# Performance work log

Measured on AMD Instinct MI355X. Metric: run time of the kernel, lower is better.

The kernel has to match this reference:

```python
import jax, jax.numpy as jnp
import numpy as np

B, CW_DIM = 256, 8192
DIM_EMBED = 128
DICT_SIZE = 4096
DIM_CODES = CW_DIM // DIM_EMBED  # 64


def setup_inputs() -> dict:
    key = jax.random.key(0)
    k1, k2 = jax.random.split(key)
    x = jax.random.normal(k1, (B, CW_DIM), dtype=jnp.float32)
    dictionary = jax.random.normal(k2, (DIM_CODES, DICT_SIZE, DIM_EMBED), dtype=jnp.float32)
    return {"x": x, "dictionary": dictionary}


def reference(x, dictionary):
    """VQVAE.quantise (eval mode): pairwise sq-distance -> argmin -> gather + one-hot.

    x: [B, cw_dim], dictionary: [C, S, E] with cw_dim = C*E.
    Returns (cw_embed [B, C*E], one_hot_idx [B, C, S]).
    """
    Bb, D = x.shape
    C, S, E = dictionary.shape
    xr = x.reshape(Bb, C, E)                                   # [B, C, E]
    x_sq = jnp.sum(xr * xr, axis=-1, keepdims=True)            # [B, C, 1]
    d_sq = jnp.sum(dictionary * dictionary, axis=-1)           # [C, S]
    cross = jnp.einsum('bce,cse->bcs', xr, dictionary)         # [B, C, S] (GEMM)
    dist = x_sq + d_sq[None, :, :] - 2.0 * cross               # [B, C, S]
    idx = jnp.argmin(dist, axis=-1)                            # [B, C]
    # gather nearest codes: dictionary[c, idx[b,c]] -> [B, C, E]
    code_ids = jnp.arange(C)[None, :]                          # [1, C]
    cw_embed = dictionary[code_ids, idx]                       # [B, C, E]
    cw_embed = cw_embed.reshape(Bb, C * E)                     # [B, cw_dim]
    one_hot_idx = jax.nn.one_hot(idx, S, dtype=x.dtype)        # [B, C, S]
    return cw_embed, one_hot_idx
```

## Files before the change

kernel.cpp:

```cpp
#include <hip/hip_runtime.h>
#include <stdint.h>


#define B_SZ 256
#define C_SZ 64
#define E_SZ 128
#define S_SZ 4096
#define CW   8192
#define LDB  136

typedef __attribute__((ext_vector_type(4))) float    float4a;
typedef __attribute__((ext_vector_type(8))) _Float16 half8;

__device__ __forceinline__ void split8(float4a f0, float4a f1, half8& hi, half8& lo) {
    #pragma unroll
    for (int j = 0; j < 4; ++j) {
        _Float16 h0 = (_Float16)f0[j];
        hi[j]     = h0;
        lo[j]     = (_Float16)(f0[j] - (float)h0);
        _Float16 h1 = (_Float16)f1[j];
        hi[4 + j] = h1;
        lo[4 + j] = (_Float16)(f1[j] - (float)h1);
    }
}

__global__ __launch_bounds__(512, 2) void argmin_mfma(
    const float* __restrict__ x,
    const float* __restrict__ dict,
    int* __restrict__ idx_out,
    float* __restrict__ cw_out)
{
    __shared__ __attribute__((aligned(16))) _Float16 bh[128 * LDB];
    __shared__ __attribute__((aligned(16))) _Float16 bl[128 * LDB];
    __shared__ float4a dsqp[128];
    __shared__ int     fid[64];
    float* rv = reinterpret_cast<float*>(bh);
    int*   ri = reinterpret_cast<int*>(bl);

    const int tid   = threadIdx.x;
    const int lane  = tid & 63;
    const int quad  = lane >> 4;
    const int l15   = lane & 15;
    const int wid   = tid >> 6;
    const int mhalf = wid & 1;
    const int nquad = wid >> 1;
    const int c     = blockIdx.x & 63;
    const int btile = blockIdx.x >> 6;

    int m_attr[4], n_attr[4];
    {
        half8 ones, enc;
        #pragma unroll
        for (int j = 0; j < 8; ++j) { ones[j] = (_Float16)1.0f; enc[j] = (_Float16)(float)l15; }
        float4a z = {0.f, 0.f, 0.f, 0.f};
        float4a pr = __builtin_amdgcn_mfma_f32_16x16x32_f16(enc, ones, z, 0, 0, 0);
        float4a pc = __builtin_amdgcn_mfma_f32_16x16x32_f16(ones, enc, z, 0, 0, 0);
        #pragma unroll
        for (int r = 0; r < 4; ++r) {
            m_attr[r] = (int)(pr[r] * 0.03125f + 0.5f);
            n_attr[r] = (int)(pc[r] * 0.03125f + 0.5f);
        }
    }

    half8 ah[2][4], al[2][4];
    #pragma unroll
    for (int mi = 0; mi < 2; ++mi) {
        int b = btile * 64 + mhalf * 32 + mi * 16 + l15;
        const float* xr = x + (size_t)b * CW + c * E_SZ;
        #pragma unroll
        for (int kk = 0; kk < 4; ++kk) {
            float4a f0 = *reinterpret_cast<const float4a*>(xr + kk * 32 + quad * 8);
            float4a f1 = *reinterpret_cast<const float4a*>(xr + kk * 32 + quad * 8 + 4);
            split8(f0, f1, ah[mi][kk], al[mi][kk]);
        }
    }

    float bestv[8];
    int   besti[8];
    #pragma unroll
    for (int i = 0; i < 8; ++i) { bestv[i] = 3.4e38f; besti[i] = 0; }

    for (int s0 = 0; s0 < S_SZ; s0 += 128) {
        __syncthreads();
        {
            int srow = tid >> 2;
            int kq   = (tid & 3) * 32;
            const float* dr = dict + ((size_t)c * S_SZ + (s0 + srow)) * E_SZ + kq;
            float dp = 0.f;
            #pragma unroll
            for (int ck = 0; ck < 4; ++ck) {
                float4a f0 = *reinterpret_cast<const float4a*>(dr + ck * 8);
                float4a f1 = *reinterpret_cast<const float4a*>(dr + ck * 8 + 4);
                half8 h, l;
                split8(f0, f1, h, l);
                #pragma unroll
                for (int j = 0; j < 4; ++j) { dp = fmaf(f0[j], f0[j], dp); dp = fmaf(f1[j], f1[j], dp); }
                *reinterpret_cast<half8*>(bh + srow * LDB + kq + ck * 8) = h;
                *reinterpret_cast<half8*>(bl + srow * LDB + kq + ck * 8) = l;
            }
            dsqp[srow][tid & 3] = dp;
        }
        __syncthreads();

        half8 bhf[2][4], blf[2][4];
        #pragma unroll
        for (int ni = 0; ni < 2; ++ni) {
            int sl = nquad * 32 + ni * 16 + l15;
            #pragma unroll
            for (int kk = 0; kk < 4; ++kk) {
                bhf[ni][kk] = *reinterpret_cast<const half8*>(bh + sl * LDB + kk * 32 + quad * 8);
                blf[ni][kk] = *reinterpret_cast<const half8*>(bl + sl * LDB + kk * 32 + quad * 8);
            }
        }

        float4a acc[2][2] = {{{0.f,0.f,0.f,0.f},{0.f,0.f,0.f,0.f}},
                             {{0.f,0.f,0.f,0.f},{0.f,0.f,0.f,0.f}}};
        #pragma unroll
        for (int kk = 0; kk < 4; ++kk)
            #pragma unroll
            for (int mi = 0; mi < 2; ++mi)
                #pragma unroll
                for (int ni = 0; ni < 2; ++ni) {
                    acc[mi][ni] = __builtin_amdgcn_mfma_f32_16x16x32_f16(
                        ah[mi][kk], bhf[ni][kk], acc[mi][ni], 0, 0, 0);
                    acc[mi][ni] = __builtin_amdgcn_mfma_f32_16x16x32_f16(
                        ah[mi][kk], blf[ni][kk], acc[mi][ni], 0, 0, 0);
                    acc[mi][ni] = __builtin_amdgcn_mfma_f32_16x16x32_f16(
                        al[mi][kk], bhf[ni][kk], acc[mi][ni], 0, 0, 0);
                }

        #pragma unroll
        for (int ni = 0; ni < 2; ++ni)
            #pragma unroll
            for (int r = 0; r < 4; ++r) {
                int sl = nquad * 32 + ni * 16 + n_attr[r];
                float4a q4 = dsqp[sl];
                float dsq = (q4[0] + q4[1]) + (q4[2] + q4[3]);
                int sg = s0 + sl;
                #pragma unroll
                for (int mi = 0; mi < 2; ++mi) {
                    float dist = dsq - 2.0f * acc[mi][ni][r];
                    int slot = mi * 4 + r;
                    if (dist < bestv[slot]) { bestv[slot] = dist; besti[slot] = sg; }
                }
            }
    }

    __syncthreads();

    #pragma unroll
    for (int mi = 0; mi < 2; ++mi)
        #pragma unroll
        for (int r = 0; r < 4; ++r) {
            int row = mhalf * 32 + mi * 16 + m_attr[r];
            int col = nquad * 16 + n_attr[r];
            rv[row * 64 + col] = bestv[mi * 4 + r];
            ri[row * 64 + col] = besti[mi * 4 + r];
        }
    __syncthreads();

    if (tid < 64) {
        float bv = 3.4e38f; int bi = 0x7fffffff;
        for (int j = 0; j < 64; ++j) {
            float v = rv[tid * 64 + j];
            int   i = ri[tid * 64 + j];
            if (v < bv || (v == bv && i < bi)) { bv = v; bi = i; }
        }
        idx_out[(btile * 64 + tid) * C_SZ + c] = bi;
        fid[tid] = bi;
    }
    __syncthreads();

    for (int u = tid; u < 64 * 32; u += 512) {
        int row = u >> 5, ch = u & 31;
        int bi = fid[row];
        float4a v = *reinterpret_cast<const float4a*>(
            dict + ((size_t)c * S_SZ + bi) * E_SZ + ch * 4);
        *reinterpret_cast<float4a*>(
            cw_out + (size_t)(btile * 64 + row) * CW + c * E_SZ + ch * 4) = v;
    }
}

__global__ void scatter_ones(const int* __restrict__ idx, float* __restrict__ oh) {
    int r = blockIdx.x * 256 + threadIdx.x;
    oh[(size_t)r * S_SZ + idx[r]] = 1.0f;
}

extern "C" void kernel_launch(void* const* d_in, const int* in_sizes, int n_in,
                              void* d_out, int out_size, void* d_ws, size_t ws_size,
                              hipStream_t stream) {
    const float* x    = (const float*)d_in[0];
    const float* dict = (const float*)d_in[1];
    float* out = (float*)d_out;
    int* idx = (int*)d_ws;
    float* oh = out + (size_t)B_SZ * CW;

    hipMemsetAsync(oh, 0, (size_t)B_SZ * C_SZ * S_SZ * sizeof(float), stream);
    argmin_mfma<<<dim3(256), dim3(512), 0, stream>>>(x, dict, idx, out);
    scatter_ones<<<dim3(B_SZ * C_SZ / 256), dim3(256), 0, stream>>>(idx, oh);
}
```

Before: 486.6 us.

## Double-buffer dictionary tiles in LDS and fuse one-hot fill into one kernel

The argmin kernel now double-buffers the fp16 hi/lo dictionary tiles in shared memory. It prefetches the next tile's global loads into registers before the MFMA work on the current tile, then splits and stores them afterwards, so each iteration needs one barrier instead of two. B-fragment loads move inside the k loop to cut register pressure. Separately, the memset plus scatter is replaced by a single kernel that writes the whole one-hot row with nontemporal vector stores, avoiding a second pass over the 256 MB output. The cost is doubled LDS use, which may reduce occupancy, and more registers held by the prefetch.

```diff
diff --git a/kernel.cpp b/kernel.cpp
--- a/kernel.cpp
+++ b/kernel.cpp
@@ -30,9 +30,9 @@
     int* __restrict__ idx_out,
     float* __restrict__ cw_out)
 {
-    __shared__ __attribute__((aligned(16))) _Float16 bh[128 * LDB];
-    __shared__ __attribute__((aligned(16))) _Float16 bl[128 * LDB];
-    __shared__ float4a dsqp[128];
+    __shared__ __attribute__((aligned(16))) _Float16 bh[2][128 * LDB];
+    __shared__ __attribute__((aligned(16))) _Float16 bl[2][128 * LDB];
+    __shared__ float4a dsqp[2][128];
     __shared__ int     fid[64];
     float* rv = reinterpret_cast<float*>(bh);
     int*   ri = reinterpret_cast<int*>(bl);
@@ -75,67 +75,87 @@
         }
     }
 
+    const int srow = tid >> 2;
+    const int kq   = (tid & 3) * 32;
+    const int q4   = tid & 3;
+    const float* drow = dict + ((size_t)c * S_SZ + srow) * E_SZ + kq;
+
+    float4a pf0[4], pf1[4];
+    #pragma unroll
+    for (int ck = 0; ck < 4; ++ck) {
+        pf0[ck] = *reinterpret_cast<const float4a*>(drow + ck * 8);
+        pf1[ck] = *reinterpret_cast<const float4a*>(drow + ck * 8 + 4);
+    }
+    {
+        float dp = 0.f;
+        #pragma unroll
+        for (int ck = 0; ck < 4; ++ck) {
+            half8 h, l;
+            split8(pf0[ck], pf1[ck], h, l);
+            #pragma unroll
+            for (int j = 0; j < 4; ++j) {
+                dp = fmaf(pf0[ck][j], pf0[ck][j], dp);
+                dp = fmaf(pf1[ck][j], pf1[ck][j], dp);
+            }
+            *reinterpret_cast<half8*>(&bh[0][srow * LDB + kq + ck * 8]) = h;
+            *reinterpret_cast<half8*>(&bl[0][srow * LDB + kq + ck * 8]) = l;
+        }
+        dsqp[0][srow][q4] = dp;
+    }
+
     float bestv[8];
     int   besti[8];
     #pragma unroll
     for (int i = 0; i < 8; ++i) { bestv[i] = 3.4e38f; besti[i] = 0; }
 
-    for (int s0 = 0; s0 < S_SZ; s0 += 128) {
-        __syncthreads();
-        {
-            int srow = tid >> 2;
-            int kq   = (tid & 3) * 32;
-            const float* dr = dict + ((size_t)c * S_SZ + (s0 + srow)) * E_SZ + kq;
-            float dp = 0.f;
+    __syncthreads();
+
+    int cur = 0;
+    for (int it = 0; it < 32; ++it) {
+        const int s0 = it * 128;
+
+        if (it + 1 < 32) {
+            const float* dr = drow + (size_t)(it + 1) * (128 * E_SZ);
             #pragma unroll
             for (int ck = 0; ck < 4; ++ck) {
-                float4a f0 = *reinterpret_cast<const float4a*>(dr + ck * 8);
-                float4a f1 = *reinterpret_cast<const float4a*>(dr + ck * 8 + 4);
-                half8 h, l;
-                split8(f0, f1, h, l);
-                #pragma unroll
-                for (int j = 0; j < 4; ++j) { dp = fmaf(f0[j], f0[j], dp); dp = fmaf(f1[j], f1[j], dp); }
-                *reinterpret_cast<half8*>(bh + srow * LDB + kq + ck * 8) = h;
-                *reinterpret_cast<half8*>(bl + srow * LDB + kq + ck * 8) = l;
-            }
-            dsqp[srow][tid & 3] = dp;
-        }
-        __syncthreads();
-
-        half8 bhf[2][4], blf[2][4];
-        #pragma unroll
-        for (int ni = 0; ni < 2; ++ni) {
-            int sl = nquad * 32 + ni * 16 + l15;
-            #pragma unroll
-            for (int kk = 0; kk < 4; ++kk) {
-                bhf[ni][kk] = *reinterpret_cast<const half8*>(bh + sl * LDB + kk * 32 + quad * 8);
-                blf[ni][kk] = *reinterpret_cast<const half8*>(bl + sl * LDB + kk * 32 + quad * 8);
-            }
-        }
-
+                pf0[ck] = *reinterpret_cast<const float4a*>(dr + ck * 8);
+                pf1[ck] = *reinterpret_cast<const float4a*>(dr + ck * 8 + 4);
+            }
+        }
+
+        const _Float16* bhc = bh[cur];
+        const _Float16* blc = bl[cur];
         float4a acc[2][2] = {{{0.f,0.f,0.f,0.f},{0.f,0.f,0.f,0.f}},
                              {{0.f,0.f,0.f,0.f},{0.f,0.f,0.f,0.f}}};
         #pragma unroll
-        for (int kk = 0; kk < 4; ++kk)
+        for (int kk = 0; kk < 4; ++kk) {
+            half8 bhf[2], blf[2];
+            #pragma unroll
+            for (int ni = 0; ni < 2; ++ni) {
+                const int sl = nquad * 32 + ni * 16 + l15;
+                bhf[ni] = *reinterpret_cast<const half8*>(bhc + sl * LDB + kk * 32 + quad * 8);
+                blf[ni] = *reinterpret_cast<const half8*>(blc + sl * LDB + kk * 32 + quad * 8);
+            }
             #pragma unroll
             for (int mi = 0; mi < 2; ++mi)
                 #pragma unroll
                 for (int ni = 0; ni < 2; ++ni) {
                     acc[mi][ni] = __builtin_amdgcn_mfma_f32_16x16x32_f16(
-                        ah[mi][kk], bhf[ni][kk], acc[mi][ni], 0, 0, 0);
+                        ah[mi][kk], bhf[ni], acc[mi][ni], 0, 0, 0);
                     acc[mi][ni] = __builtin_amdgcn_mfma_f32_16x16x32_f16(
-                        ah[mi][kk], blf[ni][kk], acc[mi][ni], 0, 0, 0);
+                        ah[mi][kk], blf[ni], acc[mi][ni], 0, 0, 0);
                     acc[mi][ni] = __builtin_amdgcn_mfma_f32_16x16x32_f16(
-                        al[mi][kk], bhf[ni][kk], acc[mi][ni], 0, 0, 0);
+                        al[mi][kk], bhf[ni], acc[mi][ni], 0, 0, 0);
                 }
+        }
 
         #pragma unroll
         for (int ni = 0; ni < 2; ++ni)
             #pragma unroll
             for (int r = 0; r < 4; ++r) {
-                int sl = nquad * 32 + ni * 16 + n_attr[r];
-                float4a q4 = dsqp[sl];
-                float dsq = (q4[0] + q4[1]) + (q4[2] + q4[3]);
+                const int sl = nquad * 32 + ni * 16 + n_attr[r];
+                float4a q4v = dsqp[cur][sl];
+                float dsq = (q4v[0] + q4v[1]) + (q4v[2] + q4v[3]);
                 int sg = s0 + sl;
                 #pragma unroll
                 for (int mi = 0; mi < 2; ++mi) {
@@ -144,9 +164,28 @@
                     if (dist < bestv[slot]) { bestv[slot] = dist; besti[slot] = sg; }
                 }
             }
-    }
-
-    __syncthreads();
+
+        if (it + 1 < 32) {
+            const int nb = cur ^ 1;
+            float dp = 0.f;
+            #pragma unroll
+            for (int ck = 0; ck < 4; ++ck) {
+                half8 h, l;
+                split8(pf0[ck], pf1[ck], h, l);
+                #pragma unroll
+                for (int j = 0; j < 4; ++j) {
+                    dp = fmaf(pf0[ck][j], pf0[ck][j], dp);
+                    dp = fmaf(pf1[ck][j], pf1[ck][j], dp);
+                }
+                *reinterpret_cast<half8*>(&bh[nb][srow * LDB + kq + ck * 8]) = h;
+                *reinterpret_cast<half8*>(&bl[nb][srow * LDB + kq + ck * 8]) = l;
+            }
+            dsqp[nb][srow][q4] = dp;
+        }
+        __syncthreads();
+        cur ^= 1;
+    }
+
 
     #pragma unroll
     for (int mi = 0; mi < 2; ++mi)
@@ -181,9 +220,20 @@
     }
 }
 
-__global__ void scatter_ones(const int* __restrict__ idx, float* __restrict__ oh) {
-    int r = blockIdx.x * 256 + threadIdx.x;
-    oh[(size_t)r * S_SZ + idx[r]] = 1.0f;
+__global__ __launch_bounds__(256) void fill_onehot(
+    const int* __restrict__ idx, float* __restrict__ oh)
+{
+    const int row = blockIdx.x;
+    const int bi  = idx[row];
+    float* base = oh + (size_t)row * S_SZ;
+    const int t = threadIdx.x;
+    #pragma unroll
+    for (int j = 0; j < 4; ++j) {
+        const int ch = j * 256 + t;
+        float4a v = {0.f, 0.f, 0.f, 0.f};
+        if ((bi >> 2) == ch) v[bi & 3] = 1.0f;
+        __builtin_nontemporal_store(v, reinterpret_cast<float4a*>(base + (size_t)ch * 4));
+    }
 }
 
 extern "C" void kernel_launch(void* const* d_in, const int* in_sizes, int n_in,
@@ -195,7 +245,6 @@
     int* idx = (int*)d_ws;
     float* oh = out + (size_t)B_SZ * CW;
 
-    hipMemsetAsync(oh, 0, (size_t)B_SZ * C_SZ * S_SZ * sizeof(float), stream);
     argmin_mfma<<<dim3(256), dim3(512), 0, stream>>>(x, dict, idx, out);
-    scatter_ones<<<dim3(B_SZ * C_SZ / 256), dim3(256), 0, stream>>>(idx, oh);
-}
+    fill_onehot<<<dim3(B_SZ * C_SZ), dim3(256), 0, stream>>>(idx, oh);
+}
```

Result: faster. 466.8 us (-4.1%).
